# Kernel tuning notes

Hardware: AMD Instinct MI355X
Metric: run time of the kernel (lower is better)

The kernel has to match this reference:

```python
import jax, jax.numpy as jnp
import numpy as np

T, B, NIN = 256, 256, 512
NH, NEMB = 512, 256


def setup_inputs() -> dict:
    key = jax.random.key(0)
    ks = jax.random.split(key, 11)
    s = 0.02  # small init to keep tanh/sigmoid in active range
    return {
        "feats": jax.random.normal(ks[0], (T, B, NIN), jnp.float32),
        "h": jax.random.normal(ks[1], (B, NH), jnp.float32),
        "cur_embed": jax.random.normal(ks[2], (B, NEMB), jnp.float32),
        # i2h: Linear(nIn, nHidden, bias=False)
        "w_i2h": jax.random.normal(ks[3], (NH, NIN), jnp.float32) * s,
        # h2h: Linear(nHidden, nHidden) with bias
        "w_h2h": jax.random.normal(ks[4], (NH, NH), jnp.float32) * s,
        "b_h2h": jax.random.normal(ks[5], (NH,), jnp.float32) * s,
        # score: Linear(nHidden, 1, bias=False)
        "w_score": jax.random.normal(ks[6], (NH,), jnp.float32) * s,
        # GRUCell(nIn + num_embeddings, nHidden); gate order r, z, n
        "w_ih": jax.random.normal(ks[7], (3 * NH, NIN + NEMB), jnp.float32) * s,
        "w_hh": jax.random.normal(ks[8], (3 * NH, NH), jnp.float32) * s,
        "b_ih": jax.random.normal(ks[9], (3 * NH,), jnp.float32) * s,
        "b_hh": jax.random.normal(ks[10], (3 * NH,), jnp.float32) * s,
    }


def reference(feats, h, cur_embed, w_i2h, w_h2h, b_h2h, w_score,
              w_ih, w_hh, b_ih, b_hh):
    # MORAN branch, test=True (FractionalPickup is skipped at eval time).
    # feats: [T, B, nIn], h: [B, nHidden], cur_embed: [B, nEmb]
    feats_ = jnp.einsum('tbc,hc->tbh', feats, w_i2h)          # i2h, [T,B,H]
    h_ = h @ w_h2h.T + b_h2h                                   # h2h, [B,H]
    emit = jnp.einsum('tbh,h->tb', jnp.tanh(feats_ + h_[None]), w_score)
    alpha = jax.nn.softmax(emit, axis=0)                       # softmax over T
    context = jnp.einsum('tb,tbc->bc', alpha, feats)           # [B,nIn]
    x = jnp.concatenate([context, cur_embed], axis=1)          # [B,nIn+nEmb]
    # GRUCell
    gi = x @ w_ih.T + b_ih                                     # [B,3H]
    gh = h @ w_hh.T + b_hh                                     # [B,3H]
    gi_r, gi_z, gi_n = jnp.split(gi, 3, axis=1)
    gh_r, gh_z, gh_n = jnp.split(gh, 3, axis=1)
    r = jax.nn.sigmoid(gi_r + gh_r)
    z = jax.nn.sigmoid(gi_z + gh_z)
    n = jnp.tanh(gi_n + r * gh_n)
    nh = (1.0 - z) * n + z * h
    return nh, alpha
```

## Files before the change

kernel.cpp:

```cpp
#include <hip/hip_runtime.h>

typedef __bf16 bf16;
typedef __bf16 bf16x4 __attribute__((ext_vector_type(4)));
typedef __bf16 bf16x8 __attribute__((ext_vector_type(8)));
typedef float  f32x4  __attribute__((ext_vector_type(4)));
typedef float  f32x16 __attribute__((ext_vector_type(16)));

#define T_DIM 256
#define B_DIM 256
#define NIN   512
#define NH    512
#define NEMB  256
#define NX    768
#define NG    1536
#define MTOT  65536

__device__ __forceinline__ float fast_tanh(float x) {
    float e = __expf(2.0f * x);
    return 1.0f - 2.0f * __builtin_amdgcn_rcpf(e + 1.0f);
}
__device__ __forceinline__ float fast_sigmoid(float x) {
    return __builtin_amdgcn_rcpf(1.0f + __expf(-x));
}

__global__ __launch_bounds__(256) void cvt_weights(
    const float* __restrict__ a0, const float* __restrict__ a1,
    const float* __restrict__ a2, const float* __restrict__ a3,
    const float* __restrict__ a4,
    bf16* __restrict__ b0, bf16* __restrict__ b1, bf16* __restrict__ b2,
    bf16* __restrict__ b3, bf16* __restrict__ b4) {
    const int N0 = 65536, N1 = 131072, N2 = 425984, N3 = 622592, N4 = 655360;
    for (int i = blockIdx.x * 256 + threadIdx.x; i < N4; i += gridDim.x * 256) {
        const float* s; bf16* d; int j; bool img = false;
        if (i < N0)      { s = a0; d = b0; j = i; img = true; }
        else if (i < N1) { s = a1; d = b1; j = i - N0; }
        else if (i < N2) { s = a2; d = b2; j = i - N1; }
        else if (i < N3) { s = a3; d = b3; j = i - N2; }
        else             { s = a4; d = b4; j = i - N3; }
        float4 v = reinterpret_cast<const float4*>(s)[j];
        bf16x4 o = { (bf16)v.x, (bf16)v.y, (bf16)v.z, (bf16)v.w };
        if (img) {
            int e = j * 4, col = e >> 9, K = e & 511;
            int g = col >> 5, cl = col & 31;
            int ks = K >> 4, kh = (K >> 3) & 1, j0 = K & 7;
            int lane = kh * 32 + cl;
            int off = (((g * 32 + ks) * 64) + lane) * 8 + j0;
            *reinterpret_cast<bf16x4*>(d + off) = o;
        } else {
            reinterpret_cast<bf16x4*>(d)[j] = o;
        }
    }
}

__global__ __launch_bounds__(256) void gemm_bias(
    const bf16* __restrict__ A, const bf16* __restrict__ B,
    const float* __restrict__ bias, float* __restrict__ C,
    int M, int N, int K) {
    __shared__ bf16 At[64][40];
    __shared__ bf16 Bt[64][40];
    const int tid = threadIdx.x;
    const int m0 = blockIdx.y * 64, n0 = blockIdx.x * 64;
    const int wid = tid >> 6, lane = tid & 63, hi = lane >> 4, lo = lane & 15;
    const int srow = tid >> 2, sseg = tid & 3;
    f32x4 acc[4] = {};

    for (int kk = 0; kk < K; kk += 32) {
        bf16x8 av = *reinterpret_cast<const bf16x8*>(A + (size_t)(m0 + srow) * K + kk + sseg * 8);
        bf16x8 bv = *reinterpret_cast<const bf16x8*>(B + (size_t)(n0 + srow) * K + kk + sseg * 8);
        __syncthreads();
        *reinterpret_cast<bf16x8*>(&At[srow][sseg * 8]) = av;
        *reinterpret_cast<bf16x8*>(&Bt[srow][sseg * 8]) = bv;
        __syncthreads();
        bf16x8 a = *reinterpret_cast<const bf16x8*>(&At[wid * 16 + lo][hi * 8]);
#pragma unroll
        for (int nt = 0; nt < 4; ++nt) {
            bf16x8 b = *reinterpret_cast<const bf16x8*>(&Bt[nt * 16 + lo][hi * 8]);
            acc[nt] = __builtin_amdgcn_mfma_f32_16x16x32_bf16(a, b, acc[nt], 0, 0, 0);
        }
    }
#pragma unroll
    for (int nt = 0; nt < 4; ++nt) {
        int n = n0 + nt * 16 + lo;
        float bv = bias[n];
#pragma unroll
        for (int r = 0; r < 4; ++r) {
            int m = m0 + wid * 16 + hi * 4 + r;
            C[(size_t)m * N + n] = acc[nt][r] + bv;
        }
    }
}

__global__ __launch_bounds__(512, 2) void emit_kernel(
    const float* __restrict__ feats, const bf16* __restrict__ Wfrag,
    const float* __restrict__ hbuf, const float* __restrict__ wscore,
    float* __restrict__ emit_part) {
    __shared__ bf16 Alds[2][32][516];
    __shared__ float ew[2][8][32];
    const int tid = threadIdx.x;
    const int wid = tid >> 6, lane = tid & 63;
    const int half = lane >> 5, l31 = lane & 31;
    const int slab = blockIdx.x & 1, mb = blockIdx.x >> 1;
    const int m0 = mb * 512;
    const int col = slab * 256 + wid * 32 + l31;

    const bf16* wsrc = Wfrag + (size_t)((slab * 8 + wid) * 32) * 512 + lane * 8;
    bf16x8 bfr[32];
#pragma unroll
    for (int ks = 0; ks < 32; ++ks)
        bfr[ks] = *reinterpret_cast<const bf16x8*>(wsrc + ks * 512);

    const float* asrc = feats + (size_t)m0 * NIN + tid * 4;
    const int awrow = tid >> 7, awcol = (tid & 127) * 4;

    float4 st[8];
#pragma unroll
    for (int j = 0; j < 8; ++j)
        st[j] = *reinterpret_cast<const float4*>(asrc + j * 2048);
#pragma unroll
    for (int j = 0; j < 8; ++j) {
        bf16x4 o = { (bf16)st[j].x, (bf16)st[j].y, (bf16)st[j].z, (bf16)st[j].w };
        *reinterpret_cast<bf16x4*>(&Alds[0][awrow + 4 * j][awcol]) = o;
    }
    __syncthreads();

    const float wsl = wscore[col];

    for (int it = 0; it < 16; ++it) {
        const int cur = it & 1;
        if (it < 15) {
            const float* an = asrc + (size_t)(it + 1) * 32 * NIN;
#pragma unroll
            for (int j = 0; j < 8; ++j)
                st[j] = *reinterpret_cast<const float4*>(an + j * 2048);
        }

        f32x16 acc0 = {}, acc1 = {};
#pragma unroll
        for (int ks = 0; ks < 32; ks += 2) {
            const bf16* ap0 = &Alds[cur][l31][ks * 16 + half * 8];
            bf16x4 p0 = *reinterpret_cast<const bf16x4*>(ap0);
            bf16x4 p1 = *reinterpret_cast<const bf16x4*>(ap0 + 4);
            bf16x8 a0 = { p0[0], p0[1], p0[2], p0[3], p1[0], p1[1], p1[2], p1[3] };
            acc0 = __builtin_amdgcn_mfma_f32_32x32x16_bf16(a0, bfr[ks], acc0, 0, 0, 0);
            const bf16* ap1 = &Alds[cur][l31][(ks + 1) * 16 + half * 8];
            bf16x4 q0 = *reinterpret_cast<const bf16x4*>(ap1);
            bf16x4 q1 = *reinterpret_cast<const bf16x4*>(ap1 + 4);
            bf16x8 a1 = { q0[0], q0[1], q0[2], q0[3], q1[0], q1[1], q1[2], q1[3] };
            acc1 = __builtin_amdgcn_mfma_f32_32x32x16_bf16(a1, bfr[ks + 1], acc1, 0, 0, 0);
        }

        float e[16];
#pragma unroll
        for (int r = 0; r < 16; ++r) {
            int row = (r & 3) + 8 * (r >> 2) + 4 * half;
            int brow = (it * 32 + row) & (B_DIM - 1);
            float x = acc0[r] + acc1[r] + hbuf[(size_t)brow * NH + col];
            e[r] = fast_tanh(x) * wsl;
        }
#pragma unroll
        for (int r = 0; r < 16; ++r)
#pragma unroll
            for (int off = 1; off < 32; off <<= 1)
                e[r] += __shfl_xor(e[r], off, 64);
        if (l31 == 0) {
#pragma unroll
            for (int r = 0; r < 16; ++r)
                ew[cur][wid][(r & 3) + 8 * (r >> 2) + 4 * half] = e[r];
        }

        if (it < 15) {
#pragma unroll
            for (int j = 0; j < 8; ++j) {
                bf16x4 o = { (bf16)st[j].x, (bf16)st[j].y, (bf16)st[j].z, (bf16)st[j].w };
                *reinterpret_cast<bf16x4*>(&Alds[cur ^ 1][awrow + 4 * j][awcol]) = o;
            }
        }
        __syncthreads();
        if (tid < 32) {
            float s = 0.0f;
#pragma unroll
            for (int w = 0; w < 8; ++w) s += ew[cur][w][tid];
            emit_part[(size_t)slab * MTOT + m0 + it * 32 + tid] = s;
        }
    }
}

__global__ __launch_bounds__(256) void softmax_t(
    const float* __restrict__ emit_part, float* __restrict__ alpha,
    float* __restrict__ out_alpha) {
    int b = blockIdx.x, t = threadIdx.x;
    int wv = t >> 6, ln = t & 63;
    size_t m = (size_t)t * B_DIM + b;
    float e = emit_part[m] + emit_part[MTOT + m];
    float mx = e;
#pragma unroll
    for (int off = 32; off; off >>= 1) mx = fmaxf(mx, __shfl_xor(mx, off, 64));
    __shared__ float red[4], red2[4];
    if (ln == 0) red[wv] = mx;
    __syncthreads();
    mx = fmaxf(fmaxf(red[0], red[1]), fmaxf(red[2], red[3]));
    float p = __expf(e - mx);
    float s = p;
#pragma unroll
    for (int off = 32; off; off >>= 1) s += __shfl_xor(s, off, 64);
    if (ln == 0) red2[wv] = s;
    __syncthreads();
    float inv = __builtin_amdgcn_rcpf(red2[0] + red2[1] + red2[2] + red2[3]);
    float a = p * inv;
    alpha[m] = a;
    out_alpha[m] = a;
}

__global__ __launch_bounds__(256) void ctx_kernel(
    const float* __restrict__ feats, const float* __restrict__ alpha,
    const float* __restrict__ emb, bf16* __restrict__ x) {
    int b = blockIdx.x;
    __shared__ float al[T_DIM];
    __shared__ float red[4][512];
    int tid = threadIdx.x;
    al[tid] = alpha[(size_t)tid * B_DIM + b];
    __syncthreads();
    int c8 = tid & 63, tq = tid >> 6;
    float acc[8] = {};
#pragma unroll 4
    for (int t = tq * 64; t < tq * 64 + 64; ++t) {
        const float* src = feats + ((size_t)(t * B_DIM + b)) * NIN + c8 * 8;
        float4 v0 = *reinterpret_cast<const float4*>(src);
        float4 v1 = *reinterpret_cast<const float4*>(src + 4);
        float a = al[t];
        acc[0] += a * v0.x; acc[1] += a * v0.y; acc[2] += a * v0.z; acc[3] += a * v0.w;
        acc[4] += a * v1.x; acc[5] += a * v1.y; acc[6] += a * v1.z; acc[7] += a * v1.w;
    }
#pragma unroll
    for (int j = 0; j < 8; ++j) red[tq][c8 * 8 + j] = acc[j];
    __syncthreads();
#pragma unroll
    for (int k = 0; k < 2; ++k) {
        int c = tid * 2 + k;
        float s = red[0][c] + red[1][c] + red[2][c] + red[3][c];
        x[(size_t)b * NX + c] = (bf16)s;
    }
    x[(size_t)b * NX + NIN + tid] = (bf16)emb[(size_t)b * NEMB + tid];
}

__global__ __launch_bounds__(256) void gru_kernel(
    const float* __restrict__ gi, const float* __restrict__ gh,
    const float* __restrict__ h, float* __restrict__ out) {
    int idx = blockIdx.x * 256 + threadIdx.x;
    int b = idx >> 9, j = idx & 511;
    const float* gib = gi + (size_t)b * NG;
    const float* ghb = gh + (size_t)b * NG;
    float r = fast_sigmoid(gib[j] + ghb[j]);
    float z = fast_sigmoid(gib[NH + j] + ghb[NH + j]);
    float n = fast_tanh(gib[2 * NH + j] + r * ghb[2 * NH + j]);
    out[idx] = (1.0f - z) * n + z * h[idx];
}

extern "C" void kernel_launch(void* const* d_in, const int* in_sizes, int n_in,
                              void* d_out, int out_size, void* d_ws, size_t ws_size,
                              hipStream_t stream) {
    const float* feats = (const float*)d_in[0];
    const float* h     = (const float*)d_in[1];
    const float* emb   = (const float*)d_in[2];
    const float* w_i2h = (const float*)d_in[3];
    const float* w_h2h = (const float*)d_in[4];
    const float* b_h2h = (const float*)d_in[5];
    const float* w_sc  = (const float*)d_in[6];
    const float* w_ih  = (const float*)d_in[7];
    const float* w_hh  = (const float*)d_in[8];
    const float* b_ih  = (const float*)d_in[9];
    const float* b_hh  = (const float*)d_in[10];
    float* out = (float*)d_out;

    char* ws = (char*)d_ws;
    bf16*  Wfrag   = (bf16*)(ws);
    bf16*  w_h2h_b = (bf16*)(ws + 524288);
    bf16*  w_ih_b  = (bf16*)(ws + 1048576);
    bf16*  w_hh_b  = (bf16*)(ws + 3407872);
    bf16*  h_b     = (bf16*)(ws + 4980736);
    bf16*  x_b     = (bf16*)(ws + 5242880);
    float* hbuf    = (float*)(ws + 5636096);
    float* emit_p  = (float*)(ws + 6160384);
    float* alpha   = (float*)(ws + 6684672);
    float* gi      = (float*)(ws + 6946816);
    float* gh      = (float*)(ws + 8519680);

    cvt_weights<<<1024, 256, 0, stream>>>(w_i2h, w_h2h, w_ih, w_hh, h,
                                          Wfrag, w_h2h_b, w_ih_b, w_hh_b, h_b);

    gemm_bias<<<dim3(8, 4), 256, 0, stream>>>(h_b, w_h2h_b, b_h2h, hbuf, 256, NH, NH);
    gemm_bias<<<dim3(24, 4), 256, 0, stream>>>(h_b, w_hh_b, b_hh, gh, 256, NG, NH);

    emit_kernel<<<256, 512, 0, stream>>>(feats, Wfrag, hbuf, w_sc, emit_p);

    softmax_t<<<256, 256, 0, stream>>>(emit_p, alpha, out + 131072);

    ctx_kernel<<<256, 256, 0, stream>>>(feats, alpha, emb, x_b);

    gemm_bias<<<dim3(24, 4), 256, 0, stream>>>(x_b, w_ih_b, b_ih, gi, 256, NG, NX);

    gru_kernel<<<512, 256, 0, stream>>>(gi, gh, h, out);
}
```

Before: 137.5 us.

## Swap MFMA operands in emit kernel so hidden dim is reduced in-lane

The emit kernel now feeds the weight fragments as the A operand and the feats tile as the B operand. The hidden dimension therefore lands on the accumulator rows, and the score reduction becomes an in-lane sum plus one cross-half shuffle instead of 16 five-step butterfly reductions. The h2h GEMM writes its output transposed so the bias-add reads are coalesced along the batch. The LDS tile switches to an XOR-swizzled unpadded layout with 128-bit reads, and the emit_part write is deferred one iteration so it falls after the barrier. Correctness depends on the swizzle and the transposed indexing matching.

```diff
diff --git a/kernel.cpp b/kernel.cpp
--- a/kernel.cpp
+++ b/kernel.cpp
@@ -55,7 +55,7 @@
 __global__ __launch_bounds__(256) void gemm_bias(
     const bf16* __restrict__ A, const bf16* __restrict__ B,
     const float* __restrict__ bias, float* __restrict__ C,
-    int M, int N, int K) {
+    int M, int N, int K, int transC) {
     __shared__ bf16 At[64][40];
     __shared__ bf16 Bt[64][40];
     const int tid = threadIdx.x;
@@ -85,103 +85,111 @@
 #pragma unroll
         for (int r = 0; r < 4; ++r) {
             int m = m0 + wid * 16 + hi * 4 + r;
-            C[(size_t)m * N + n] = acc[nt][r] + bv;
+            if (transC) C[(size_t)n * M + m] = acc[nt][r] + bv;
+            else        C[(size_t)m * N + n] = acc[nt][r] + bv;
         }
     }
 }
 
 __global__ __launch_bounds__(512, 2) void emit_kernel(
     const float* __restrict__ feats, const bf16* __restrict__ Wfrag,
-    const float* __restrict__ hbuf, const float* __restrict__ wscore,
+    const float* __restrict__ hT, const float* __restrict__ wscore,
     float* __restrict__ emit_part) {
-    __shared__ bf16 Alds[2][32][516];
+    __shared__ bf16 Alds[2][32 * 512];
     __shared__ float ew[2][8][32];
     const int tid = threadIdx.x;
     const int wid = tid >> 6, lane = tid & 63;
     const int half = lane >> 5, l31 = lane & 31;
-    const int slab = blockIdx.x & 1, mb = blockIdx.x >> 1;
-    const int m0 = mb * 512;
-    const int col = slab * 256 + wid * 32 + l31;
+    const int slab = blockIdx.x & 1, mchunk = blockIdx.x >> 1;
+    const size_t m0 = (size_t)mchunk * 512;
+    const int n0w = slab * 256 + wid * 32;
 
     const bf16* wsrc = Wfrag + (size_t)((slab * 8 + wid) * 32) * 512 + lane * 8;
-    bf16x8 bfr[32];
+    bf16x8 wfr[32];
 #pragma unroll
     for (int ks = 0; ks < 32; ++ks)
-        bfr[ks] = *reinterpret_cast<const bf16x8*>(wsrc + ks * 512);
-
-    const float* asrc = feats + (size_t)m0 * NIN + tid * 4;
-    const int awrow = tid >> 7, awcol = (tid & 127) * 4;
-
-    float4 st[8];
-#pragma unroll
-    for (int j = 0; j < 8; ++j)
-        st[j] = *reinterpret_cast<const float4*>(asrc + j * 2048);
-#pragma unroll
-    for (int j = 0; j < 8; ++j) {
-        bf16x4 o = { (bf16)st[j].x, (bf16)st[j].y, (bf16)st[j].z, (bf16)st[j].w };
-        *reinterpret_cast<bf16x4*>(&Alds[0][awrow + 4 * j][awcol]) = o;
-    }
-    __syncthreads();
-
-    const float wsl = wscore[col];
-
+        wfr[ks] = *reinterpret_cast<const bf16x8*>(wsrc + ks * 512);
+
+    float wsr[16];
+#pragma unroll
+    for (int r = 0; r < 16; ++r)
+        wsr[r] = wscore[n0w + (r & 3) + 8 * (r >> 2) + 4 * half];
+
+    const int sr = tid >> 6, scc = tid & 63;
+    const float* abase = feats + (m0 + sr) * NIN + scc * 8;
+    const int adst = ((scc ^ sr) << 3);
+
+    float4 va[8];
+#pragma unroll
+    for (int i = 0; i < 4; ++i) {
+        const float* p = abase + (size_t)i * 8 * NIN;
+        va[2 * i]     = *reinterpret_cast<const float4*>(p);
+        va[2 * i + 1] = *reinterpret_cast<const float4*>(p + 4);
+    }
+#pragma unroll
+    for (int i = 0; i < 4; ++i) {
+        bf16x8 o = { (bf16)va[2*i].x, (bf16)va[2*i].y, (bf16)va[2*i].z, (bf16)va[2*i].w,
+                     (bf16)va[2*i+1].x, (bf16)va[2*i+1].y, (bf16)va[2*i+1].z, (bf16)va[2*i+1].w };
+        *reinterpret_cast<bf16x8*>(&Alds[0][(i * 8 + sr) * 512 + adst]) = o;
+    }
+    __syncthreads();
+
+    const int arow = l31 * 512, axor = (l31 & 7);
     for (int it = 0; it < 16; ++it) {
         const int cur = it & 1;
         if (it < 15) {
-            const float* an = asrc + (size_t)(it + 1) * 32 * NIN;
-#pragma unroll
-            for (int j = 0; j < 8; ++j)
-                st[j] = *reinterpret_cast<const float4*>(an + j * 2048);
+#pragma unroll
+            for (int i = 0; i < 4; ++i) {
+                const float* p = abase + (size_t)((it + 1) * 32 + i * 8) * NIN;
+                va[2 * i]     = *reinterpret_cast<const float4*>(p);
+                va[2 * i + 1] = *reinterpret_cast<const float4*>(p + 4);
+            }
+        }
+        if (it > 0 && tid < 32) {
+            float s = 0.0f;
+#pragma unroll
+            for (int w = 0; w < 8; ++w) s += ew[cur ^ 1][w][tid];
+            emit_part[(size_t)slab * MTOT + m0 + (it - 1) * 32 + tid] = s;
         }
 
         f32x16 acc0 = {}, acc1 = {};
+        const bf16* ab = &Alds[cur][0];
 #pragma unroll
         for (int ks = 0; ks < 32; ks += 2) {
-            const bf16* ap0 = &Alds[cur][l31][ks * 16 + half * 8];
-            bf16x4 p0 = *reinterpret_cast<const bf16x4*>(ap0);
-            bf16x4 p1 = *reinterpret_cast<const bf16x4*>(ap0 + 4);
-            bf16x8 a0 = { p0[0], p0[1], p0[2], p0[3], p1[0], p1[1], p1[2], p1[3] };
-            acc0 = __builtin_amdgcn_mfma_f32_32x32x16_bf16(a0, bfr[ks], acc0, 0, 0, 0);
-            const bf16* ap1 = &Alds[cur][l31][(ks + 1) * 16 + half * 8];
-            bf16x4 q0 = *reinterpret_cast<const bf16x4*>(ap1);
-            bf16x4 q1 = *reinterpret_cast<const bf16x4*>(ap1 + 4);
-            bf16x8 a1 = { q0[0], q0[1], q0[2], q0[3], q1[0], q1[1], q1[2], q1[3] };
-            acc1 = __builtin_amdgcn_mfma_f32_32x32x16_bf16(a1, bfr[ks + 1], acc1, 0, 0, 0);
-        }
-
-        float e[16];
+            bf16x8 f0 = *reinterpret_cast<const bf16x8*>(
+                ab + arow + (((2 * ks + half) ^ axor) << 3));
+            acc0 = __builtin_amdgcn_mfma_f32_32x32x16_bf16(wfr[ks], f0, acc0, 0, 0, 0);
+            bf16x8 f1 = *reinterpret_cast<const bf16x8*>(
+                ab + arow + (((2 * ks + 2 + half) ^ axor) << 3));
+            acc1 = __builtin_amdgcn_mfma_f32_32x32x16_bf16(wfr[ks + 1], f1, acc1, 0, 0, 0);
+        }
+
+        float e = 0.0f;
+        const int bcol = (it * 32 + l31) & (B_DIM - 1);
 #pragma unroll
         for (int r = 0; r < 16; ++r) {
-            int row = (r & 3) + 8 * (r >> 2) + 4 * half;
-            int brow = (it * 32 + row) & (B_DIM - 1);
-            float x = acc0[r] + acc1[r] + hbuf[(size_t)brow * NH + col];
-            e[r] = fast_tanh(x) * wsl;
-        }
-#pragma unroll
-        for (int r = 0; r < 16; ++r)
-#pragma unroll
-            for (int off = 1; off < 32; off <<= 1)
-                e[r] += __shfl_xor(e[r], off, 64);
-        if (l31 == 0) {
-#pragma unroll
-            for (int r = 0; r < 16; ++r)
-                ew[cur][wid][(r & 3) + 8 * (r >> 2) + 4 * half] = e[r];
-        }
+            int nr = (r & 3) + 8 * (r >> 2) + 4 * half;
+            float hv = hT[(size_t)(n0w + nr) * B_DIM + bcol];
+            e += fast_tanh(acc0[r] + acc1[r] + hv) * wsr[r];
+        }
+        e += __shfl_xor(e, 32, 64);
+        if (lane < 32) ew[cur][wid][l31] = e;
 
         if (it < 15) {
 #pragma unroll
-            for (int j = 0; j < 8; ++j) {
-                bf16x4 o = { (bf16)st[j].x, (bf16)st[j].y, (bf16)st[j].z, (bf16)st[j].w };
-                *reinterpret_cast<bf16x4*>(&Alds[cur ^ 1][awrow + 4 * j][awcol]) = o;
+            for (int i = 0; i < 4; ++i) {
+                bf16x8 o = { (bf16)va[2*i].x, (bf16)va[2*i].y, (bf16)va[2*i].z, (bf16)va[2*i].w,
+                             (bf16)va[2*i+1].x, (bf16)va[2*i+1].y, (bf16)va[2*i+1].z, (bf16)va[2*i+1].w };
+                *reinterpret_cast<bf16x8*>(&Alds[cur ^ 1][(i * 8 + sr) * 512 + adst]) = o;
             }
         }
         __syncthreads();
-        if (tid < 32) {
-            float s = 0.0f;
-#pragma unroll
-            for (int w = 0; w < 8; ++w) s += ew[cur][w][tid];
-            emit_part[(size_t)slab * MTOT + m0 + it * 32 + tid] = s;
-        }
+    }
+    if (tid < 32) {
+        float s = 0.0f;
+#pragma unroll
+        for (int w = 0; w < 8; ++w) s += ew[1][w][tid];
+        emit_part[(size_t)slab * MTOT + m0 + 15 * 32 + tid] = s;
     }
 }
 
@@ -279,7 +287,7 @@
     bf16*  w_hh_b  = (bf16*)(ws + 3407872);
     bf16*  h_b     = (bf16*)(ws + 4980736);
     bf16*  x_b     = (bf16*)(ws + 5242880);
-    float* hbuf    = (float*)(ws + 5636096);
+    float* hT      = (float*)(ws + 5636096);
     float* emit_p  = (float*)(ws + 6160384);
     float* alpha   = (float*)(ws + 6684672);
     float* gi      = (float*)(ws + 6946816);
@@ -288,16 +296,16 @@
     cvt_weights<<<1024, 256, 0, stream>>>(w_i2h, w_h2h, w_ih, w_hh, h,
                                           Wfrag, w_h2h_b, w_ih_b, w_hh_b, h_b);
 
-    gemm_bias<<<dim3(8, 4), 256, 0, stream>>>(h_b, w_h2h_b, b_h2h, hbuf, 256, NH, NH);
-    gemm_bias<<<dim3(24, 4), 256, 0, stream>>>(h_b, w_hh_b, b_hh, gh, 256, NG, NH);
-
-    emit_kernel<<<256, 512, 0, stream>>>(feats, Wfrag, hbuf, w_sc, emit_p);
+    gemm_bias<<<dim3(8, 4), 256, 0, stream>>>(h_b, w_h2h_b, b_h2h, hT, 256, NH, NH, 1);
+    gemm_bias<<<dim3(24, 4), 256, 0, stream>>>(h_b, w_hh_b, b_hh, gh, 256, NG, NH, 0);
+
+    emit_kernel<<<256, 512, 0, stream>>>(feats, Wfrag, hT, w_sc, emit_p);
 
     softmax_t<<<256, 256, 0, stream>>>(emit_p, alpha, out + 131072);
 
     ctx_kernel<<<256, 256, 0, stream>>>(feats, alpha, emb, x_b);
 
-    gemm_bias<<<dim3(24, 4), 256, 0, stream>>>(x_b, w_ih_b, b_ih, gi, 256, NG, NX);
+    gemm_bias<<<dim3(24, 4), 256, 0, stream>>>(x_b, w_ih_b, b_ih, gi, 256, NG, NX, 0);
 
     gru_kernel<<<512, 256, 0, stream>>>(gi, gh, h, out);
 }
```

Result: slower. 227.1 us (+65.2%).
